# Kernel optimization log

Hardware: AMD Instinct MI355X
Metric: run time of the kernel (lower is better)

The kernel has to match this reference:

```python
import jax, jax.numpy as jnp
import numpy as np

HEAD_DIM = 64

def setup_inputs() -> dict:
    key = jax.random.key(0)
    ks = jax.random.split(key, 6)
    b, q_len, kv_len, emb, h, d = 4, 2048, 2048, 1024, 16, HEAD_DIM
    scale = 1.0 / np.sqrt(emb)  # fan_in variance scaling for stable logits
    return {
        "inputs_q": jax.random.normal(ks[0], (b, q_len, emb), jnp.float32),
        "inputs_kv": jax.random.normal(ks[1], (b, kv_len, emb), jnp.float32),
        "Wq": jax.random.normal(ks[2], (emb, h, d), jnp.float32) * scale,
        "Wk": jax.random.normal(ks[3], (emb, h, d), jnp.float32) * scale,
        "Wv": jax.random.normal(ks[4], (emb, h, d), jnp.float32) * scale,
        "Wo": jax.random.normal(ks[5], (h, d, emb), jnp.float32) * scale,
    }

def reference(inputs_q, inputs_kv, Wq, Wk, Wv, Wo):
    # QKV projections; query kernel init includes 1/sqrt(head_dim) in the
    depth_scale = jnp.sqrt(jnp.asarray(HEAD_DIM, inputs_q.dtype))
    q = jnp.einsum('bqe,ehd->bqhd', inputs_q, Wq) / depth_scale
    k = jnp.einsum('bke,ehd->bkhd', inputs_kv, Wk)
    v = jnp.einsum('bke,ehd->bkhd', inputs_kv, Wv)
    # full attention: einsum -> softmax -> einsum (naive, materializes bhqk)
    attn_weights = jnp.einsum('bqhd,bkhd->bhqk', q, k)
    attn_weights = jax.nn.softmax(attn_weights, axis=-1)
    out = jnp.einsum('bhqk,bkhd->bqhd', attn_weights, v)
    # output projection over (heads, head_dim)
    return jnp.einsum('bqhd,hde->bqe', out, Wo)
```

## Files before the change

### kernel.cpp

```cpp
#include <hip/hip_runtime.h>
#include <hip/hip_bf16.h>


typedef __attribute__((ext_vector_type(8))) short bf16x8;
typedef __attribute__((ext_vector_type(4))) float f32x4;
typedef __attribute__((ext_vector_type(16))) float f32x16;

#define MFMA16(a, b, c) __builtin_amdgcn_mfma_f32_16x16x32_bf16((a), (b), (c), 0, 0, 0)
#define MFMA32(a, b, c) __builtin_amdgcn_mfma_f32_32x32x16_bf16((a), (b), (c), 0, 0, 0)

__device__ __forceinline__ short f2bf(float f) {
  union { float f; unsigned u; } v; v.f = f;
  unsigned r = v.u + 0x7fffu + ((v.u >> 16) & 1u);
  return (short)(r >> 16);
}

__device__ __forceinline__ unsigned cvtpk(float lo, float hi) {
  unsigned r;
  asm("v_cvt_pk_bf16_f32 %0, %1, %2" : "=v"(r) : "v"(lo), "v"(hi));
  return r;
}

__device__ __forceinline__ void plswap(unsigned& a, unsigned& b) {
  asm volatile("v_permlane32_swap_b32 %0, %1" : "+v"(a), "+v"(b));
}

__device__ __forceinline__ void gld16(const short* g, short* l) {
  __builtin_amdgcn_global_load_lds(
      (const __attribute__((address_space(1))) unsigned int*)g,
      (__attribute__((address_space(3))) unsigned int*)l, 16, 0, 0);
}

__global__ __launch_bounds__(256) void wtrans_kernel(
    const float* __restrict__ w0, const float* __restrict__ w1,
    const float* __restrict__ w2, const float* __restrict__ w3,
    short* __restrict__ out) {
  __shared__ float t[32][33];
  const int z = blockIdx.z;
  const float* src = (z == 0) ? w0 : (z == 1) ? w1 : (z == 2) ? w2 : w3;
  short* dst = out + (size_t)z * (1024 * 1024);
  const int x = threadIdx.x & 31, y = threadIdx.x >> 5;
  const int n0 = blockIdx.x * 32, k0 = blockIdx.y * 32;
#pragma unroll
  for (int yy = y; yy < 32; yy += 8)
    t[yy][x] = src[(size_t)(k0 + yy) * 1024 + n0 + x];
  __syncthreads();
#pragma unroll
  for (int yy = y; yy < 32; yy += 8)
    dst[(size_t)(n0 + yy) * 1024 + k0 + x] = f2bf(t[x][yy]);
}

template <bool AF32, bool BF32, bool OUTF32>
__global__ __launch_bounds__(256) void gemm_kk(
    const void* __restrict__ Ap, const void* __restrict__ Bp,
    void* __restrict__ Cp, int M, int N, int K, int ldc, float scale) {
  __shared__ __align__(16) short At[128][88];
  __shared__ __align__(16) short Bt[128][88];
  const int tid = threadIdx.x;
  const int l = tid & 63;
  const int w = tid >> 6;
  const int wm = (w >> 1) * 64, wn = (w & 1) * 64;
  const int m0 = blockIdx.y * 128, n0 = blockIdx.x * 128;
  const int srow = tid >> 3, scol = (tid & 7) * 8;

  f32x4 acc[4][4];
#pragma unroll
  for (int i = 0; i < 4; ++i)
#pragma unroll
    for (int j = 0; j < 4; ++j) acc[i][j] = (f32x4){0.f, 0.f, 0.f, 0.f};

  for (int k0 = 0; k0 < K; k0 += 64) {
    __syncthreads();
#pragma unroll
    for (int c = 0; c < 4; ++c) {
      const int r = srow + c * 32;
      if (AF32) {
        const float* s = (const float*)Ap + (size_t)(m0 + r) * K + k0 + scol;
        const float4 f0 = *(const float4*)s;
        const float4 f1 = *(const float4*)(s + 4);
        bf16x8 v;
        v[0] = f2bf(f0.x); v[1] = f2bf(f0.y); v[2] = f2bf(f0.z); v[3] = f2bf(f0.w);
        v[4] = f2bf(f1.x); v[5] = f2bf(f1.y); v[6] = f2bf(f1.z); v[7] = f2bf(f1.w);
        *(bf16x8*)&At[r][scol] = v;
      } else {
        const short* s = (const short*)Ap + (size_t)(m0 + r) * K + k0 + scol;
        *(bf16x8*)&At[r][scol] = *(const bf16x8*)s;
      }
      if (BF32) {
        const float* s = (const float*)Bp + (size_t)(n0 + r) * K + k0 + scol;
        const float4 f0 = *(const float4*)s;
        const float4 f1 = *(const float4*)(s + 4);
        bf16x8 v;
        v[0] = f2bf(f0.x); v[1] = f2bf(f0.y); v[2] = f2bf(f0.z); v[3] = f2bf(f0.w);
        v[4] = f2bf(f1.x); v[5] = f2bf(f1.y); v[6] = f2bf(f1.z); v[7] = f2bf(f1.w);
        *(bf16x8*)&Bt[r][scol] = v;
      } else {
        const short* s = (const short*)Bp + (size_t)(n0 + r) * K + k0 + scol;
        *(bf16x8*)&Bt[r][scol] = *(const bf16x8*)s;
      }
    }
    __syncthreads();
#pragma unroll
    for (int ks = 0; ks < 2; ++ks) {
      bf16x8 af[4], bfr[4];
#pragma unroll
      for (int mt = 0; mt < 4; ++mt)
        af[mt] = *(const bf16x8*)&At[wm + mt * 16 + (l & 15)][ks * 32 + (l >> 4) * 8];
#pragma unroll
      for (int nt = 0; nt < 4; ++nt)
        bfr[nt] = *(const bf16x8*)&Bt[wn + nt * 16 + (l & 15)][ks * 32 + (l >> 4) * 8];
#pragma unroll
      for (int mt = 0; mt < 4; ++mt)
#pragma unroll
        for (int nt = 0; nt < 4; ++nt)
          acc[mt][nt] = MFMA16(af[mt], bfr[nt], acc[mt][nt]);
    }
  }
#pragma unroll
  for (int mt = 0; mt < 4; ++mt)
#pragma unroll
    for (int nt = 0; nt < 4; ++nt)
#pragma unroll
      for (int r = 0; r < 4; ++r) {
        const int row = m0 + wm + mt * 16 + (l >> 4) * 4 + r;
        const int col = n0 + wn + nt * 16 + (l & 15);
        const float v = acc[mt][nt][r] * scale;
        if (OUTF32)
          ((float*)Cp)[(size_t)row * ldc + col] = v;
        else
          ((short*)Cp)[(size_t)row * ldc + col] = f2bf(v);
      }
}

__global__ __launch_bounds__(256) void attn32_kernel(
    const short* __restrict__ qb, const short* __restrict__ kb,
    const short* __restrict__ vT, short* __restrict__ ob) {
  __shared__ __align__(16) short Ksh[2][64][64];
  __shared__ __align__(16) short Vsh[2][64][64];
  const int tid = threadIdx.x, w = tid >> 6, l = tid & 63;
  const int hi = l >> 5, ln = l & 31;
  const int bh = blockIdx.y, b = bh >> 4, h = bh & 15;
  const size_t bL = (size_t)b * 2048;
  const int hd = h * 64;
  const int q0 = blockIdx.x * 128 + w * 32;

  const int sr0 = w * 8 + (l >> 3);
  const int sc0 = ((l & 7) ^ (sr0 & 7)) << 3;

#define STAGE(BUF, KV0)                                                      \
  do {                                                                       \
    gld16(kb + (bL + (KV0) + sr0) * 1024 + hd + sc0, &Ksh[BUF][w * 8][0]);   \
    gld16(kb + (bL + (KV0) + sr0 + 32) * 1024 + hd + sc0,                    \
          &Ksh[BUF][32 + w * 8][0]);                                         \
    gld16(vT + (size_t)(hd + sr0) * 8192 + bL + (KV0) + sc0,                 \
          &Vsh[BUF][w * 8][0]);                                              \
    gld16(vT + (size_t)(hd + sr0 + 32) * 8192 + bL + (KV0) + sc0,            \
          &Vsh[BUF][32 + w * 8][0]);                                         \
  } while (0)

  bf16x8 qf[4];
  {
    const short* qrow = qb + (bL + q0 + ln) * 1024 + hd + hi * 8;
#pragma unroll
    for (int c = 0; c < 4; ++c) qf[c] = *(const bf16x8*)(qrow + c * 16);
  }

  f32x16 o0, o1;
#pragma unroll
  for (int i = 0; i < 16; ++i) { o0[i] = 0.f; o1[i] = 0.f; }
  float m = -1e30f, lsum = 0.f;

  const int swz = ln & 7;

  STAGE(0, 0);
  int cur = 0;
  for (int t = 0; t < 32; ++t) {
    __syncthreads();
    if (t < 31) STAGE(cur ^ 1, (t + 1) * 64);

    f32x16 s0, s1;
#pragma unroll
    for (int i = 0; i < 16; ++i) { s0[i] = 0.f; s1[i] = 0.f; }
#pragma unroll
    for (int c = 0; c < 4; ++c) {
      const int bcol = ((((c << 1) | hi)) ^ swz) << 3;
      const bf16x8 kf0 = *(const bf16x8*)&Ksh[cur][ln][bcol];
      const bf16x8 kf1 = *(const bf16x8*)&Ksh[cur][32 + ln][bcol];
      s0 = MFMA32(kf0, qf[c], s0);
      s1 = MFMA32(kf1, qf[c], s1);
    }

    float pmax = s0[0];
#pragma unroll
    for (int i = 1; i < 16; ++i) pmax = fmaxf(pmax, s0[i]);
#pragma unroll
    for (int i = 0; i < 16; ++i) pmax = fmaxf(pmax, s1[i]);
    pmax = fmaxf(pmax, __shfl_xor(pmax, 32));
    const float mnew = fmaxf(m, pmax);
    const float fac = exp2f(m - mnew);
    m = mnew;
    float p0[16], p1[16];
    float sum = 0.f;
#pragma unroll
    for (int i = 0; i < 16; ++i) { p0[i] = exp2f(s0[i] - m); sum += p0[i]; }
#pragma unroll
    for (int i = 0; i < 16; ++i) { p1[i] = exp2f(s1[i] - m); sum += p1[i]; }
    sum += __shfl_xor(sum, 32);
    lsum = lsum * fac + sum;
#pragma unroll
    for (int i = 0; i < 16; ++i) { o0[i] *= fac; o1[i] *= fac; }

#define PVCHUNK(PARR, BASE, C)                                               \
  do {                                                                       \
    unsigned A0 = cvtpk(PARR[(BASE) + 0], PARR[(BASE) + 1]);                 \
    unsigned A1 = cvtpk(PARR[(BASE) + 2], PARR[(BASE) + 3]);                 \
    unsigned B0 = cvtpk(PARR[(BASE) + 4], PARR[(BASE) + 5]);                 \
    unsigned B1 = cvtpk(PARR[(BASE) + 6], PARR[(BASE) + 7]);                 \
    plswap(A0, B0);                                                          \
    plswap(A1, B1);                                                          \
    union { unsigned u[4]; bf16x8 v; } pf;                                   \
    pf.u[0] = A0; pf.u[1] = A1; pf.u[2] = B0; pf.u[3] = B1;                  \
    const int bcol = ((((C) << 1) | hi) ^ swz) << 3;                         \
    const bf16x8 vf0 = *(const bf16x8*)&Vsh[cur][ln][bcol];                  \
    const bf16x8 vf1 = *(const bf16x8*)&Vsh[cur][32 + ln][bcol];             \
    o0 = MFMA32(vf0, pf.v, o0);                                              \
    o1 = MFMA32(vf1, pf.v, o1);                                              \
  } while (0)

    PVCHUNK(p0, 0, 0);
    PVCHUNK(p0, 8, 1);
    PVCHUNK(p1, 0, 2);
    PVCHUNK(p1, 8, 3);
#undef PVCHUNK

    cur ^= 1;
  }

  const float inv = 1.0f / lsum;
  short* orow = ob + (bL + q0 + ln) * 1024 + hd + hi * 4;
#pragma unroll
  for (int g = 0; g < 4; ++g) {
    const unsigned a0 = cvtpk(o0[4 * g + 0] * inv, o0[4 * g + 1] * inv);
    const unsigned a1 = cvtpk(o0[4 * g + 2] * inv, o0[4 * g + 3] * inv);
    *(uint2*)(orow + 8 * g) = make_uint2(a0, a1);
    const unsigned b0 = cvtpk(o1[4 * g + 0] * inv, o1[4 * g + 1] * inv);
    const unsigned b1 = cvtpk(o1[4 * g + 2] * inv, o1[4 * g + 3] * inv);
    *(uint2*)(orow + 32 + 8 * g) = make_uint2(b0, b1);
  }
#undef STAGE
}

extern "C" void kernel_launch(void* const* d_in, const int* in_sizes, int n_in,
                              void* d_out, int out_size, void* d_ws,
                              size_t ws_size, hipStream_t stream) {
  const size_t ML = (size_t)8192 * 1024;
  short* qb = (short*)d_ws;
  short* kb = qb + ML;
  short* vT = kb + ML;
  short* ob = vT + ML;
  short* wT = ob + ML;
  short* WqT = wT;
  short* WkT = wT + (size_t)1024 * 1024;
  short* WvT = wT + (size_t)2 * 1024 * 1024;
  short* WoT = wT + (size_t)3 * 1024 * 1024;

  wtrans_kernel<<<dim3(32, 32, 4), 256, 0, stream>>>(
      (const float*)d_in[2], (const float*)d_in[3], (const float*)d_in[4],
      (const float*)d_in[5], wT);

  gemm_kk<true, false, false><<<dim3(8, 64), 256, 0, stream>>>(
      d_in[0], WqT, qb, 8192, 1024, 1024, 1024, 0.125f * 1.44269504f);
  gemm_kk<true, false, false><<<dim3(8, 64), 256, 0, stream>>>(
      d_in[1], WkT, kb, 8192, 1024, 1024, 1024, 1.0f);
  gemm_kk<false, true, false><<<dim3(64, 8), 256, 0, stream>>>(
      WvT, d_in[1], vT, 1024, 8192, 1024, 8192, 1.0f);

  attn32_kernel<<<dim3(16, 64), 256, 0, stream>>>(qb, kb, vT, ob);

  gemm_kk<false, false, true><<<dim3(8, 64), 256, 0, stream>>>(
      ob, WoT, d_out, 8192, 1024, 1024, 1024, 1.0f);
}
```

Baseline: 295.6 us.

## Pre-cast activations to bf16 and load GEMM tiles via global_load_lds

Adds a standalone fp32-to-bf16 cast kernel for both input activations, reusing free workspace buffers. All GEMMs then take bf16 operands and stage tiles directly into LDS with global_load_lds instead of register round-trips. The LDS tiles lose their padding, which may add bank conflicts on fragment reads. Separately, the attention kernel raises wave priority around its MFMA sections to favour matrix issue.

```diff
diff --git a/kernel.cpp b/kernel.cpp
--- a/kernel.cpp
+++ b/kernel.cpp
@@ -29,6 +29,20 @@
   __builtin_amdgcn_global_load_lds(
       (const __attribute__((address_space(1))) unsigned int*)g,
       (__attribute__((address_space(3))) unsigned int*)l, 16, 0, 0);
+}
+
+__global__ __launch_bounds__(256) void cast_kernel(
+    const float* __restrict__ in, short* __restrict__ out, int n8) {
+  int i = blockIdx.x * 256 + threadIdx.x;
+  const int stride = gridDim.x * 256;
+  for (; i < n8; i += stride) {
+    const float4 f0 = ((const float4*)in)[2 * i];
+    const float4 f1 = ((const float4*)in)[2 * i + 1];
+    bf16x8 v;
+    v[0] = f2bf(f0.x); v[1] = f2bf(f0.y); v[2] = f2bf(f0.z); v[3] = f2bf(f0.w);
+    v[4] = f2bf(f1.x); v[5] = f2bf(f1.y); v[6] = f2bf(f1.z); v[7] = f2bf(f1.w);
+    ((bf16x8*)out)[i] = v;
+  }
 }
 
 __global__ __launch_bounds__(256) void wtrans_kernel(
@@ -50,18 +64,17 @@
     dst[(size_t)(n0 + yy) * 1024 + k0 + x] = f2bf(t[x][yy]);
 }
 
-template <bool AF32, bool BF32, bool OUTF32>
-__global__ __launch_bounds__(256) void gemm_kk(
-    const void* __restrict__ Ap, const void* __restrict__ Bp,
+template <bool OUTF32>
+__global__ __launch_bounds__(256) void gemm_bb(
+    const short* __restrict__ A, const short* __restrict__ B,
     void* __restrict__ Cp, int M, int N, int K, int ldc, float scale) {
-  __shared__ __align__(16) short At[128][88];
-  __shared__ __align__(16) short Bt[128][88];
-  const int tid = threadIdx.x;
-  const int l = tid & 63;
-  const int w = tid >> 6;
+  __shared__ __align__(16) short At[128][64];
+  __shared__ __align__(16) short Bt[128][64];
+  const int tid = threadIdx.x, l = tid & 63, w = tid >> 6;
   const int wm = (w >> 1) * 64, wn = (w & 1) * 64;
   const int m0 = blockIdx.y * 128, n0 = blockIdx.x * 128;
-  const int srow = tid >> 3, scol = (tid & 7) * 8;
+  const short* Abase = A + (size_t)(m0 + w * 8 + (l >> 3)) * K + (l & 7) * 8;
+  const short* Bbase = B + (size_t)(n0 + w * 8 + (l >> 3)) * K + (l & 7) * 8;
 
   f32x4 acc[4][4];
 #pragma unroll
@@ -72,32 +85,9 @@
   for (int k0 = 0; k0 < K; k0 += 64) {
     __syncthreads();
 #pragma unroll
-    for (int c = 0; c < 4; ++c) {
-      const int r = srow + c * 32;
-      if (AF32) {
-        const float* s = (const float*)Ap + (size_t)(m0 + r) * K + k0 + scol;
-        const float4 f0 = *(const float4*)s;
-        const float4 f1 = *(const float4*)(s + 4);
-        bf16x8 v;
-        v[0] = f2bf(f0.x); v[1] = f2bf(f0.y); v[2] = f2bf(f0.z); v[3] = f2bf(f0.w);
-        v[4] = f2bf(f1.x); v[5] = f2bf(f1.y); v[6] = f2bf(f1.z); v[7] = f2bf(f1.w);
-        *(bf16x8*)&At[r][scol] = v;
-      } else {
-        const short* s = (const short*)Ap + (size_t)(m0 + r) * K + k0 + scol;
-        *(bf16x8*)&At[r][scol] = *(const bf16x8*)s;
-      }
-      if (BF32) {
-        const float* s = (const float*)Bp + (size_t)(n0 + r) * K + k0 + scol;
-        const float4 f0 = *(const float4*)s;
-        const float4 f1 = *(const float4*)(s + 4);
-        bf16x8 v;
-        v[0] = f2bf(f0.x); v[1] = f2bf(f0.y); v[2] = f2bf(f0.z); v[3] = f2bf(f0.w);
-        v[4] = f2bf(f1.x); v[5] = f2bf(f1.y); v[6] = f2bf(f1.z); v[7] = f2bf(f1.w);
-        *(bf16x8*)&Bt[r][scol] = v;
-      } else {
-        const short* s = (const short*)Bp + (size_t)(n0 + r) * K + k0 + scol;
-        *(bf16x8*)&Bt[r][scol] = *(const bf16x8*)s;
-      }
+    for (int i = 0; i < 4; ++i) {
+      gld16(Abase + (size_t)i * 32 * K + k0, &At[i * 32 + w * 8][0]);
+      gld16(Bbase + (size_t)i * 32 * K + k0, &Bt[i * 32 + w * 8][0]);
     }
     __syncthreads();
 #pragma unroll
@@ -181,6 +171,7 @@
     f32x16 s0, s1;
 #pragma unroll
     for (int i = 0; i < 16; ++i) { s0[i] = 0.f; s1[i] = 0.f; }
+    __builtin_amdgcn_s_setprio(1);
 #pragma unroll
     for (int c = 0; c < 4; ++c) {
       const int bcol = ((((c << 1) | hi)) ^ swz) << 3;
@@ -189,6 +180,7 @@
       s0 = MFMA32(kf0, qf[c], s0);
       s1 = MFMA32(kf1, qf[c], s1);
     }
+    __builtin_amdgcn_s_setprio(0);
 
     float pmax = s0[0];
 #pragma unroll
@@ -210,6 +202,7 @@
 #pragma unroll
     for (int i = 0; i < 16; ++i) { o0[i] *= fac; o1[i] *= fac; }
 
+    __builtin_amdgcn_s_setprio(1);
 #define PVCHUNK(PARR, BASE, C)                                               \
   do {                                                                       \
     unsigned A0 = cvtpk(PARR[(BASE) + 0], PARR[(BASE) + 1]);                 \
@@ -232,6 +225,7 @@
     PVCHUNK(p1, 0, 2);
     PVCHUNK(p1, 8, 3);
 #undef PVCHUNK
+    __builtin_amdgcn_s_setprio(0);
 
     cur ^= 1;
   }
@@ -263,20 +257,27 @@
   short* WkT = wT + (size_t)1024 * 1024;
   short* WvT = wT + (size_t)2 * 1024 * 1024;
   short* WoT = wT + (size_t)3 * 1024 * 1024;
+  short* qibf = vT;
+  short* kvbf = ob;
 
   wtrans_kernel<<<dim3(32, 32, 4), 256, 0, stream>>>(
       (const float*)d_in[2], (const float*)d_in[3], (const float*)d_in[4],
       (const float*)d_in[5], wT);
 
-  gemm_kk<true, false, false><<<dim3(8, 64), 256, 0, stream>>>(
-      d_in[0], WqT, qb, 8192, 1024, 1024, 1024, 0.125f * 1.44269504f);
-  gemm_kk<true, false, false><<<dim3(8, 64), 256, 0, stream>>>(
-      d_in[1], WkT, kb, 8192, 1024, 1024, 1024, 1.0f);
-  gemm_kk<false, true, false><<<dim3(64, 8), 256, 0, stream>>>(
-      WvT, d_in[1], vT, 1024, 8192, 1024, 8192, 1.0f);
+  cast_kernel<<<2048, 256, 0, stream>>>((const float*)d_in[0], qibf,
+                                        (int)(ML / 8));
+  cast_kernel<<<2048, 256, 0, stream>>>((const float*)d_in[1], kvbf,
+                                        (int)(ML / 8));
+
+  gemm_bb<false><<<dim3(8, 64), 256, 0, stream>>>(
+      qibf, WqT, qb, 8192, 1024, 1024, 1024, 0.125f * 1.44269504f);
+  gemm_bb<false><<<dim3(8, 64), 256, 0, stream>>>(
+      kvbf, WkT, kb, 8192, 1024, 1024, 1024, 1.0f);
+  gemm_bb<false><<<dim3(64, 8), 256, 0, stream>>>(
+      WvT, kvbf, vT, 1024, 8192, 1024, 8192, 1.0f);
 
   attn32_kernel<<<dim3(16, 64), 256, 0, stream>>>(qb, kb, vT, ob);
 
-  gemm_kk<false, false, true><<<dim3(8, 64), 256, 0, stream>>>(
+  gemm_bb<true><<<dim3(8, 64), 256, 0, stream>>>(
       ob, WoT, d_out, 8192, 1024, 1024, 1024, 1.0f);
 }
```

After: 274.7 us. 1.08x faster.
